# Optimization experiments

Hardware: AMD Instinct MI355X
Metric: run time of the kernel (lower is better)

## Reference

```python
import jax, jax.numpy as jnp
import numpy as np

D_MODEL = 1024
N_HEADS = 16
NUM_EXPERTS = 8
GATE_HIDDEN = 128
B, T = 4, 2048


def setup_inputs() -> dict:
    key = jax.random.key(0)
    ks = jax.random.split(key, 14)
    s = 0.02
    d, e, gh = D_MODEL, NUM_EXPERTS, GATE_HIDDEN
    return {
        "hidden_states": jax.random.normal(ks[0], (B, T, d), jnp.float32),
        # torch Linear weights are [out_features, in_features]
        "Wq": jax.random.normal(ks[1], (e, d, d), jnp.float32) * s,
        "bq": jax.random.normal(ks[2], (e, d), jnp.float32) * s,
        "Wk": jax.random.normal(ks[3], (e, d, d), jnp.float32) * s,
        "bk": jax.random.normal(ks[4], (e, d), jnp.float32) * s,
        "Wv": jax.random.normal(ks[5], (e, d, d), jnp.float32) * s,
        "bv": jax.random.normal(ks[6], (e, d), jnp.float32) * s,
        "Wg1": jax.random.normal(ks[7], (gh, d), jnp.float32) * s,
        "bg1": jax.random.normal(ks[8], (gh,), jnp.float32) * s,
        "Wg2": jax.random.normal(ks[9], (e, gh), jnp.float32) * s,
        "bg2": jax.random.normal(ks[10], (e,), jnp.float32) * s,
        "Wo": jax.random.normal(ks[11], (d, d), jnp.float32) * s,
        "bo": jax.random.normal(ks[12], (d,), jnp.float32) * s,
    }


def reference(hidden_states, Wq, bq, Wk, bk, Wv, bv, Wg1, bg1, Wg2, bg2, Wo, bo):
    Bb, Tt, C = hidden_states.shape
    H = N_HEADS
    Dh = C // H

    # Per-sample gating over mean-pooled sequence
    pooled = hidden_states.mean(axis=1)                        # [B, C]
    gate_h = jax.nn.relu(pooled @ Wg1.T + bg1)                 # [B, 128]
    gw = jax.nn.softmax(gate_h @ Wg2.T + bg2, axis=-1)         # [B, E]

    # Since gating weights are per-batch scalars, sum_e w_e * (x W_e^T + b_e)
    # == x (sum_e w_e W_e)^T + sum_e w_e b_e  — same math, one GEMM per sample.
    def proj(We, be):
        W_eff = jnp.einsum('be,eoi->boi', gw, We)              # [B, C, C]
        b_eff = gw @ be                                        # [B, C]
        y = jnp.einsum('bti,boi->bto', hidden_states, W_eff) + b_eff[:, None, :]
        return y.reshape(Bb, Tt, H, Dh).transpose(0, 2, 1, 3)  # [B, H, T, Dh]

    q = proj(Wq, bq)
    k = proj(Wk, bk)
    v = proj(Wv, bv)

    scores = jnp.einsum('bhtd,bhsd->bhts', q, k) / (Dh ** 0.5)
    attn = jax.nn.softmax(scores, axis=-1)                     # dropout is inference identity
    out = jnp.einsum('bhts,bhsd->bhtd', attn, v)
    out = out.transpose(0, 2, 1, 3).reshape(Bb, Tt, C)
    return out @ Wo.T + bo
```

## Files before the change

### kernel.cpp

```cpp
#include <hip/hip_runtime.h>

#define B_ 4
#define T_ 2048
#define C_ 1024
#define H_ 16
#define DH_ 64
#define E_ 8
#define GH_ 128

typedef unsigned short bf16_t;
typedef __attribute__((ext_vector_type(8))) __bf16 bf16x8;
typedef __attribute__((ext_vector_type(2))) __bf16 bf16x2;
typedef __attribute__((ext_vector_type(4))) float floatx4;

#if __has_builtin(__builtin_amdgcn_exp2f)
#define EXP2F(x) __builtin_amdgcn_exp2f(x)
#else
#define EXP2F(x) exp2f(x)
#endif

__device__ __forceinline__ bf16_t f2bf(float f) {
  unsigned int u = __builtin_bit_cast(unsigned int, f);
  u += 0x7fffu + ((u >> 16) & 1u);
  return (bf16_t)(u >> 16);
}
__device__ __forceinline__ void async16(const void* g, void* l) {
  __builtin_amdgcn_global_load_lds(
      (const __attribute__((address_space(1))) unsigned int*)g,
      (__attribute__((address_space(3))) unsigned int*)l, 16, 0, 0);
}

__global__ void cvt_kernel(const float* __restrict__ src, bf16_t* __restrict__ dst) {
  int i = (blockIdx.x * 256 + threadIdx.x) * 4;
  float4 v = *(const float4*)(src + i);
  bf16_t o4[4] = {f2bf(v.x), f2bf(v.y), f2bf(v.z), f2bf(v.w)};
  *(uint2*)(dst + i) = *(const uint2*)o4;
}

__global__ void pool_kernel(const float* __restrict__ x, float* __restrict__ partial) {
  int bz = blockIdx.x;
  int b = bz >> 4;
  int r0 = (bz & 15) * 128;
  int t = threadIdx.x;
  float a0 = 0.f, a1 = 0.f, a2 = 0.f, a3 = 0.f;
  const float* xb = x + (size_t)b * T_ * C_ + (size_t)r0 * C_;
  for (int r = 0; r < 128; ++r) {
    const float* row = xb + (size_t)r * C_;
    a0 += row[t]; a1 += row[t + 256]; a2 += row[t + 512]; a3 += row[t + 768];
  }
  float* p = partial + (size_t)bz * C_;
  p[t] = a0; p[t + 256] = a1; p[t + 512] = a2; p[t + 768] = a3;
}

__global__ void gate_kernel(const float* __restrict__ partial,
                            const float* __restrict__ Wg1, const float* __restrict__ bg1,
                            const float* __restrict__ Wg2, const float* __restrict__ bg2,
                            const float* __restrict__ bq, const float* __restrict__ bk,
                            const float* __restrict__ bv,
                            float* __restrict__ gw, float* __restrict__ beff) {
  int b = blockIdx.x;
  int t = threadIdx.x;
  __shared__ float spool[C_];
  __shared__ float sh[GH_];
  __shared__ float sgw[E_];
  for (int i = t; i < C_; i += GH_) {
    float s = 0.f;
    for (int j = 0; j < 16; ++j) s += partial[(size_t)(b * 16 + j) * C_ + i];
    spool[i] = s * (1.0f / T_);
  }
  __syncthreads();
  {
    float acc = 0.f;
    const float* wr = Wg1 + (size_t)t * C_;
    for (int i = 0; i < C_; i += 4) {
      float4 w = *(const float4*)(wr + i);
      acc += spool[i] * w.x + spool[i + 1] * w.y + spool[i + 2] * w.z + spool[i + 3] * w.w;
    }
    acc += bg1[t];
    sh[t] = fmaxf(acc, 0.0f);
  }
  __syncthreads();
  if (t < E_) {
    float acc = 0.f;
    const float* wr = Wg2 + t * GH_;
    for (int j = 0; j < GH_; ++j) acc += sh[j] * wr[j];
    sgw[t] = acc + bg2[t];
  }
  __syncthreads();
  if (t == 0) {
    float mx = sgw[0];
    for (int e = 1; e < E_; ++e) mx = fmaxf(mx, sgw[e]);
    float s = 0.f, ex[E_];
    for (int e = 0; e < E_; ++e) { ex[e] = __expf(sgw[e] - mx); s += ex[e]; }
    float inv = 1.0f / s;
    for (int e = 0; e < E_; ++e) { sgw[e] = ex[e] * inv; gw[b * E_ + e] = sgw[e]; }
  }
  __syncthreads();
  for (int o = t; o < C_; o += GH_) {
    float aq = 0.f, ak = 0.f, av = 0.f;
    #pragma unroll
    for (int e = 0; e < E_; ++e) {
      float w = sgw[e];
      aq += w * bq[e * C_ + o];
      ak += w * bk[e * C_ + o];
      av += w * bv[e * C_ + o];
    }
    beff[(0 * B_ + b) * C_ + o] = aq;
    beff[(1 * B_ + b) * C_ + o] = ak;
    beff[(2 * B_ + b) * C_ + o] = av;
  }
}

__global__ void combine_kernel(const float* __restrict__ Wq, const float* __restrict__ Wk,
                               const float* __restrict__ Wv, const float* __restrict__ gw,
                               bf16_t* __restrict__ Weff) {
  int g = blockIdx.x * 256 + threadIdx.x;
  int ig = (g & 127) * 8;
  int o = (g >> 7) & 1023;
  int p = g >> 17;
  const float* W = (p == 0) ? Wq : (p == 1) ? Wk : Wv;
  const float* src = W + (size_t)o * C_ + ig;
  float acc[B_][8];
  #pragma unroll
  for (int b = 0; b < B_; ++b)
    #pragma unroll
    for (int j = 0; j < 8; ++j) acc[b][j] = 0.f;
  #pragma unroll
  for (int e = 0; e < E_; ++e) {
    float4 lo = *(const float4*)(src + (size_t)e * C_ * C_);
    float4 hi = *(const float4*)(src + (size_t)e * C_ * C_ + 4);
    float w8[8] = {lo.x, lo.y, lo.z, lo.w, hi.x, hi.y, hi.z, hi.w};
    #pragma unroll
    for (int b = 0; b < B_; ++b) {
      float wgt = gw[b * E_ + e];
      #pragma unroll
      for (int j = 0; j < 8; ++j) acc[b][j] += wgt * w8[j];
    }
  }
  #pragma unroll
  for (int b = 0; b < B_; ++b) {
    bf16_t out8[8];
    #pragma unroll
    for (int j = 0; j < 8; ++j) out8[j] = f2bf(acc[b][j]);
    *(uint4*)(Weff + ((size_t)p * B_ + b) * C_ * C_ + (size_t)o * C_ + ig) = *(const uint4*)out8;
  }
}

template <int MODE>
__global__ __launch_bounds__(256) void gemm128(const bf16_t* __restrict__ X,
                                               const bf16_t* __restrict__ W,
                                               const float* __restrict__ bias,
                                               bf16_t* __restrict__ Yb,
                                               float* __restrict__ Yf) {
  if (MODE == 0) {
    int z = blockIdx.z;
    X += (size_t)(z & 3) * (T_ * C_);
    W += (size_t)z * (C_ * C_);
    bias += (size_t)z * C_;
    Yb += (size_t)z * (T_ * C_);
  }
  const int n0 = blockIdx.x * 128;
  const int m0 = blockIdx.y * 128;

  __shared__ __align__(16) bf16_t As[128][64];
  __shared__ __align__(16) bf16_t Bs[128][64];

  const int tid = threadIdx.x;
  const int wave = tid >> 6;
  const int lane = tid & 63;
  const int quad = lane >> 4;
  const int l16 = lane & 15;
  const int wm = (wave & 1) * 64;
  const int wn = (wave >> 1) * 64;

  floatx4 acc[4][4];
  #pragma unroll
  for (int i = 0; i < 4; ++i)
    #pragma unroll
    for (int j = 0; j < 4; ++j) { floatx4 zz = {0.f, 0.f, 0.f, 0.f}; acc[i][j] = zz; }

  const int ar = tid >> 3;
  const int ac = (tid & 7) * 8;
  const bf16_t* Xp = X + (size_t)(m0 + ar) * C_ + ac;
  const bf16_t* Wp = W + (size_t)(n0 + ar) * C_ + ac;

  for (int k0 = 0; k0 < C_; k0 += 64) {
    __syncthreads();
    #pragma unroll
    for (int s = 0; s < 4; ++s) {
      async16(Xp + (size_t)(s * 32) * C_ + k0, &As[ar + s * 32][ac]);
      async16(Wp + (size_t)(s * 32) * C_ + k0, &Bs[ar + s * 32][ac]);
    }
    __syncthreads();
    #pragma unroll
    for (int kk = 0; kk < 64; kk += 32) {
      bf16x8 af[4], bfr[4];
      #pragma unroll
      for (int i = 0; i < 4; ++i) {
        af[i] = *(const bf16x8*)(&As[wm + i * 16 + l16][kk + quad * 8]);
        bfr[i] = *(const bf16x8*)(&Bs[wn + i * 16 + l16][kk + quad * 8]);
      }
      #pragma unroll
      for (int mi = 0; mi < 4; ++mi)
        #pragma unroll
        for (int ni = 0; ni < 4; ++ni)
          acc[mi][ni] = __builtin_amdgcn_mfma_f32_16x16x32_bf16(af[mi], bfr[ni], acc[mi][ni], 0, 0, 0);
    }
  }

  #pragma unroll
  for (int mi = 0; mi < 4; ++mi) {
    #pragma unroll
    for (int ni = 0; ni < 4; ++ni) {
      const int n = n0 + wn + ni * 16 + l16;
      const float bv = bias[n];
      #pragma unroll
      for (int r = 0; r < 4; ++r) {
        const int m = m0 + wm + mi * 16 + quad * 4 + r;
        float v = acc[mi][ni][r] + bv;
        if (MODE == 0) Yb[((size_t)(n >> 6) * T_ + m) * DH_ + (n & 63)] = f2bf(v);
        else           Yf[(size_t)m * C_ + n] = v;
      }
    }
  }
}

__global__ void vtrans_kernel(const bf16_t* __restrict__ qkv, bf16_t* __restrict__ Vt) {
  const int kt = blockIdx.x;
  const int bh = blockIdx.y;
  const int b = bh >> 4, h = bh & 15;
  const bf16_t* src = qkv + (size_t)(8 + b) * T_ * C_ + (size_t)h * T_ * DH_ + (size_t)kt * 64 * DH_;
  __shared__ __align__(16) bf16_t L[64][64];
  const int t = threadIdx.x;
  const int r = t >> 2;
  const int c = (t & 3) * 16;
  const int sw = r & 48;
  *(uint4*)(&L[r][c ^ sw]) = *(const uint4*)(src + (size_t)r * DH_ + c);
  *(uint4*)(&L[r][(c ^ sw) + 8]) = *(const uint4*)(src + (size_t)r * DH_ + c + 8);
  __syncthreads();
  const int sw2 = c & 48;
  bf16_t tmp[16];
  #pragma unroll
  for (int j = 0; j < 16; ++j) tmp[j] = L[c + j][r ^ sw2];
  bf16_t* dst = Vt + (size_t)bh * DH_ * T_ + (size_t)r * T_ + (size_t)kt * 64 + c;
  *(uint4*)(dst) = *(const uint4*)(tmp);
  *(uint4*)(dst + 8) = *(const uint4*)(tmp + 8);
}

__global__ __launch_bounds__(512, 4) void attn_kernel(const bf16_t* __restrict__ qkv,
                                                      const bf16_t* __restrict__ Vt,
                                                      bf16_t* __restrict__ out) {
  const int bh = blockIdx.x;
  const int qt = blockIdx.y;
  const int b = bh >> 4, h = bh & 15;
  const __bf16* Q = (const __bf16*)(qkv + (size_t)b * T_ * C_ + (size_t)h * T_ * DH_);
  const bf16_t* Kp = qkv + (size_t)(4 + b) * T_ * C_ + (size_t)h * T_ * DH_;
  const bf16_t* Vtb = Vt + (size_t)bh * DH_ * T_;

  __shared__ __align__(16) bf16_t Ks[512 * 8];
  __shared__ __align__(16) bf16_t Vs[512 * 8];
  __shared__ __align__(16) __bf16 Ps[128][72];

  const int tid = threadIdx.x;
  const int wave = tid >> 6;
  const int lane = tid & 63;
  const int quad = lane >> 4;
  const int l16 = lane & 15;

  const float QSC = 0.125f * 1.44269504f;
  bf16x8 qb[2];
  {
    const __bf16* qrow = Q + (size_t)(qt * 128 + wave * 16 + l16) * DH_;
    #pragma unroll
    for (int kc = 0; kc < 2; ++kc) {
      union { bf16x8 v; __bf16 e[8]; } fr;
      #pragma unroll
      for (int j = 0; j < 8; ++j) fr.e[j] = (__bf16)((float)qrow[kc * 32 + quad * 8 + j] * QSC);
      qb[kc] = fr.v;
    }
  }

  int kaoff[2][4];
  int vboff[2][4];
  #pragma unroll
  for (int kc = 0; kc < 2; ++kc) {
    #pragma unroll
    for (int i = 0; i < 4; ++i) {
      int row = i * 16 + l16;
      int off = ((row << 3) + (((kc << 2) + quad) ^ (row & 7))) * 8;
      kaoff[kc][i] = off;
      vboff[kc][i] = off;
    }
  }
  __bf16* prow = &Ps[wave * 16 + l16][0];
  const bf16x8* paptr0 = (const bf16x8*)(prow + 0 * 32 + quad * 8);
  const bf16x8* paptr1 = (const bf16x8*)(prow + 1 * 32 + quad * 8);

  floatx4 oacc[4];
  #pragma unroll
  for (int di = 0; di < 4; ++di) { floatx4 zz = {0.f, 0.f, 0.f, 0.f}; oacc[di] = zz; }
  float lrun = 0.f;

  const int srow = tid >> 3;
  const int schk = (tid & 7) ^ (srow & 7);

  for (int kt = 0; kt < T_ / 64; ++kt) {
    const int kv0 = kt * 64;
    __syncthreads();
    async16(Kp + (size_t)(kv0 + srow) * DH_ + schk * 8, Ks + (size_t)tid * 8);
    async16(Vtb + (size_t)srow * T_ + kv0 + schk * 8, Vs + (size_t)tid * 8);
    __syncthreads();

    floatx4 s_[4];
    #pragma unroll
    for (int ni = 0; ni < 4; ++ni) { floatx4 zz = {0.f, 0.f, 0.f, 0.f}; s_[ni] = zz; }
    #pragma unroll
    for (int kc = 0; kc < 2; ++kc) {
      #pragma unroll
      for (int ni = 0; ni < 4; ++ni) {
        bf16x8 ka = *(const bf16x8*)(Ks + kaoff[kc][ni]);
        s_[ni] = __builtin_amdgcn_mfma_f32_16x16x32_bf16(ka, qb[kc], s_[ni], 0, 0, 0);
      }
    }

    float lsum = 0.f;
    #pragma unroll
    for (int ni = 0; ni < 4; ++ni) {
      float p0 = EXP2F(s_[ni][0]);
      float p1 = EXP2F(s_[ni][1]);
      float p2 = EXP2F(s_[ni][2]);
      float p3 = EXP2F(s_[ni][3]);
      lsum += (p0 + p1) + (p2 + p3);
      bf16x2 w0 = {(__bf16)p0, (__bf16)p1};
      bf16x2 w1 = {(__bf16)p2, (__bf16)p3};
      uint2 pk;
      pk.x = __builtin_bit_cast(unsigned int, w0);
      pk.y = __builtin_bit_cast(unsigned int, w1);
      *(uint2*)(prow + ni * 16 + quad * 4) = pk;
    }
    lsum += __shfl_xor(lsum, 16);
    lsum += __shfl_xor(lsum, 32);
    lrun += lsum;

    #pragma unroll
    for (int kc = 0; kc < 2; ++kc) {
      bf16x8 pa = *(kc == 0 ? paptr0 : paptr1);
      #pragma unroll
      for (int di = 0; di < 4; ++di) {
        bf16x8 vb = *(const bf16x8*)(Vs + vboff[kc][di]);
        oacc[di] = __builtin_amdgcn_mfma_f32_16x16x32_bf16(pa, vb, oacc[di], 0, 0, 0);
      }
    }
  }

  float linv = 1.0f / lrun;
  #pragma unroll
  for (int r = 0; r < 4; ++r) {
    float li = __shfl(linv, quad * 20 + r);
    int m = qt * 128 + wave * 16 + quad * 4 + r;
    #pragma unroll
    for (int di = 0; di < 4; ++di) {
      int d = di * 16 + l16;
      out[(size_t)b * T_ * C_ + (size_t)m * C_ + h * DH_ + d] = f2bf(oacc[di][r] * li);
    }
  }
}

extern "C" void kernel_launch(void* const* d_in, const int* in_sizes, int n_in,
                              void* d_out, int out_size, void* d_ws, size_t ws_size,
                              hipStream_t stream) {
  (void)in_sizes; (void)n_in; (void)out_size; (void)ws_size;
  const float* x   = (const float*)d_in[0];
  const float* Wq  = (const float*)d_in[1];
  const float* bq  = (const float*)d_in[2];
  const float* Wk  = (const float*)d_in[3];
  const float* bk  = (const float*)d_in[4];
  const float* Wv  = (const float*)d_in[5];
  const float* bv  = (const float*)d_in[6];
  const float* Wg1 = (const float*)d_in[7];
  const float* bg1 = (const float*)d_in[8];
  const float* Wg2 = (const float*)d_in[9];
  const float* bg2 = (const float*)d_in[10];
  const float* Wo  = (const float*)d_in[11];
  const float* bo  = (const float*)d_in[12];

  char* ws = (char*)d_ws;
  size_t off = 0;
  auto alloc = [&](size_t bytes) -> void* {
    void* p = ws + off;
    off += (bytes + 255) & ~(size_t)255;
    return p;
  };
  float* partial = (float*)alloc((size_t)B_ * 16 * C_ * 4);
  float* gw      = (float*)alloc((size_t)B_ * E_ * 4);
  float* beff    = (float*)alloc((size_t)3 * B_ * C_ * 4);
  bf16_t* xbf    = (bf16_t*)alloc((size_t)B_ * T_ * C_ * 2);
  bf16_t* Wobf   = (bf16_t*)alloc((size_t)C_ * C_ * 2);
  bf16_t* Weff   = (bf16_t*)alloc((size_t)3 * B_ * C_ * C_ * 2);
  bf16_t* qkv    = (bf16_t*)alloc((size_t)3 * B_ * T_ * C_ * 2);
  bf16_t* attn   = (bf16_t*)alloc((size_t)B_ * T_ * C_ * 2);
  bf16_t* Vt = xbf;

  pool_kernel<<<dim3(B_ * 16), 256, 0, stream>>>(x, partial);
  gate_kernel<<<dim3(B_), GH_, 0, stream>>>(partial, Wg1, bg1, Wg2, bg2,
                                            bq, bk, bv, gw, beff);
  combine_kernel<<<dim3(3 * C_ * (C_ / 8) / 256), 256, 0, stream>>>(Wq, Wk, Wv, gw, Weff);
  cvt_kernel<<<dim3((B_ * T_ * C_) / 1024), 256, 0, stream>>>(x, xbf);
  cvt_kernel<<<dim3((C_ * C_) / 1024), 256, 0, stream>>>(Wo, Wobf);
  gemm128<0><<<dim3(C_ / 128, T_ / 128, 12), 256, 0, stream>>>(xbf, Weff, beff, qkv, nullptr);
  vtrans_kernel<<<dim3(T_ / 64, B_ * H_), 256, 0, stream>>>(qkv, Vt);
  attn_kernel<<<dim3(B_ * H_, T_ / 128), 512, 0, stream>>>(qkv, Vt, attn);
  gemm128<1><<<dim3(C_ / 128, (B_ * T_) / 128, 1), 256, 0, stream>>>(attn, Wobf, bo, nullptr, (float*)d_out);
}
```

Measured before the change: 450.7 us.

## Double-buffer K/V tiles in attention with async prefetch and wave priority

The attention kernel now keeps two LDS buffers for K and V and issues the async load of the next 64-key tile before computing on the current one, waiting with s_waitcnt vmcnt instead of a full sync. The goal is to hide global-load latency behind the MFMA and softmax work. It also raises wave priority around the MFMA sections and changes the launch bounds to 6 blocks per CU. The extra LDS and the occupancy hint may pressure registers or LDS capacity, so fewer blocks could actually fit per CU.

```diff
diff --git a/kernel.cpp b/kernel.cpp
--- a/kernel.cpp
+++ b/kernel.cpp
@@ -247,7 +247,7 @@
   *(uint4*)(dst + 8) = *(const uint4*)(tmp + 8);
 }
 
-__global__ __launch_bounds__(512, 4) void attn_kernel(const bf16_t* __restrict__ qkv,
+__global__ __launch_bounds__(512, 6) void attn_kernel(const bf16_t* __restrict__ qkv,
                                                       const bf16_t* __restrict__ Vt,
                                                       bf16_t* __restrict__ out) {
   const int bh = blockIdx.x;
@@ -257,8 +257,8 @@
   const bf16_t* Kp = qkv + (size_t)(4 + b) * T_ * C_ + (size_t)h * T_ * DH_;
   const bf16_t* Vtb = Vt + (size_t)bh * DH_ * T_;
 
-  __shared__ __align__(16) bf16_t Ks[512 * 8];
-  __shared__ __align__(16) bf16_t Vs[512 * 8];
+  __shared__ __align__(16) bf16_t Ks[2][4096];
+  __shared__ __align__(16) bf16_t Vs[2][4096];
   __shared__ __align__(16) __bf16 Ps[128][72];
 
   const int tid = threadIdx.x;
@@ -280,16 +280,13 @@
     }
   }
 
-  int kaoff[2][4];
-  int vboff[2][4];
+  int off_[2][4];
   #pragma unroll
   for (int kc = 0; kc < 2; ++kc) {
     #pragma unroll
     for (int i = 0; i < 4; ++i) {
       int row = i * 16 + l16;
-      int off = ((row << 3) + (((kc << 2) + quad) ^ (row & 7))) * 8;
-      kaoff[kc][i] = off;
-      vboff[kc][i] = off;
+      off_[kc][i] = ((row << 3) + (((kc << 2) + quad) ^ (row & 7))) * 8;
     }
   }
   __bf16* prow = &Ps[wave * 16 + l16][0];
@@ -303,55 +300,91 @@
 
   const int srow = tid >> 3;
   const int schk = (tid & 7) ^ (srow & 7);
-
-  for (int kt = 0; kt < T_ / 64; ++kt) {
-    const int kv0 = kt * 64;
-    __syncthreads();
-    async16(Kp + (size_t)(kv0 + srow) * DH_ + schk * 8, Ks + (size_t)tid * 8);
-    async16(Vtb + (size_t)srow * T_ + kv0 + schk * 8, Vs + (size_t)tid * 8);
-    __syncthreads();
-
-    floatx4 s_[4];
-    #pragma unroll
-    for (int ni = 0; ni < 4; ++ni) { floatx4 zz = {0.f, 0.f, 0.f, 0.f}; s_[ni] = zz; }
-    #pragma unroll
-    for (int kc = 0; kc < 2; ++kc) {
-      #pragma unroll
-      for (int ni = 0; ni < 4; ++ni) {
-        bf16x8 ka = *(const bf16x8*)(Ks + kaoff[kc][ni]);
-        s_[ni] = __builtin_amdgcn_mfma_f32_16x16x32_bf16(ka, qb[kc], s_[ni], 0, 0, 0);
-      }
-    }
-
-    float lsum = 0.f;
-    #pragma unroll
-    for (int ni = 0; ni < 4; ++ni) {
-      float p0 = EXP2F(s_[ni][0]);
-      float p1 = EXP2F(s_[ni][1]);
-      float p2 = EXP2F(s_[ni][2]);
-      float p3 = EXP2F(s_[ni][3]);
-      lsum += (p0 + p1) + (p2 + p3);
-      bf16x2 w0 = {(__bf16)p0, (__bf16)p1};
-      bf16x2 w1 = {(__bf16)p2, (__bf16)p3};
-      uint2 pk;
-      pk.x = __builtin_bit_cast(unsigned int, w0);
-      pk.y = __builtin_bit_cast(unsigned int, w1);
-      *(uint2*)(prow + ni * 16 + quad * 4) = pk;
-    }
-    lsum += __shfl_xor(lsum, 16);
-    lsum += __shfl_xor(lsum, 32);
-    lrun += lsum;
-
-    #pragma unroll
-    for (int kc = 0; kc < 2; ++kc) {
-      bf16x8 pa = *(kc == 0 ? paptr0 : paptr1);
-      #pragma unroll
-      for (int di = 0; di < 4; ++di) {
-        bf16x8 vb = *(const bf16x8*)(Vs + vboff[kc][di]);
-        oacc[di] = __builtin_amdgcn_mfma_f32_16x16x32_bf16(pa, vb, oacc[di], 0, 0, 0);
-      }
-    }
-  }
+  const bf16_t* kg = Kp + (size_t)srow * DH_ + schk * 8;
+  const bf16_t* vg = Vtb + (size_t)srow * T_ + schk * 8;
+
+#define STAGE(BUF) do {                                   \
+    async16(kg, &Ks[BUF][tid * 8]);                       \
+    async16(vg, &Vs[BUF][tid * 8]);                       \
+    kg += 64 * DH_;                                       \
+    vg += 64;                                             \
+  } while (0)
+
+#define WAITV(N) asm volatile("s_waitcnt vmcnt(" #N ")" ::: "memory")
+#define BAR() __builtin_amdgcn_s_barrier()
+
+#define COMPUTE(CUR) do {                                                            \
+    floatx4 s_[4];                                                                   \
+    _Pragma("unroll")                                                                \
+    for (int ni = 0; ni < 4; ++ni) { floatx4 zz = {0.f, 0.f, 0.f, 0.f}; s_[ni] = zz; } \
+    __builtin_amdgcn_s_setprio(1);                                                   \
+    _Pragma("unroll")                                                                \
+    for (int kc = 0; kc < 2; ++kc) {                                                 \
+      _Pragma("unroll")                                                              \
+      for (int ni = 0; ni < 4; ++ni) {                                               \
+        bf16x8 ka = *(const bf16x8*)(&Ks[CUR][off_[kc][ni]]);                        \
+        s_[ni] = __builtin_amdgcn_mfma_f32_16x16x32_bf16(ka, qb[kc], s_[ni], 0, 0, 0); \
+      }                                                                              \
+    }                                                                                \
+    __builtin_amdgcn_s_setprio(0);                                                   \
+    float lsum = 0.f;                                                                \
+    _Pragma("unroll")                                                                \
+    for (int ni = 0; ni < 4; ++ni) {                                                 \
+      float p0 = EXP2F(s_[ni][0]);                                                   \
+      float p1 = EXP2F(s_[ni][1]);                                                   \
+      float p2 = EXP2F(s_[ni][2]);                                                   \
+      float p3 = EXP2F(s_[ni][3]);                                                   \
+      lsum += (p0 + p1) + (p2 + p3);                                                 \
+      bf16x2 w0 = {(__bf16)p0, (__bf16)p1};                                          \
+      bf16x2 w1 = {(__bf16)p2, (__bf16)p3};                                          \
+      uint2 pk;                                                                      \
+      pk.x = __builtin_bit_cast(unsigned int, w0);                                   \
+      pk.y = __builtin_bit_cast(unsigned int, w1);                                   \
+      *(uint2*)(prow + ni * 16 + quad * 4) = pk;                                     \
+    }                                                                                \
+    lsum += __shfl_xor(lsum, 16);                                                    \
+    lsum += __shfl_xor(lsum, 32);                                                    \
+    lrun += lsum;                                                                    \
+    __builtin_amdgcn_s_setprio(1);                                                   \
+    _Pragma("unroll")                                                                \
+    for (int kc = 0; kc < 2; ++kc) {                                                 \
+      bf16x8 pa = *(kc == 0 ? paptr0 : paptr1);                                      \
+      _Pragma("unroll")                                                              \
+      for (int di = 0; di < 4; ++di) {                                               \
+        bf16x8 vb = *(const bf16x8*)(&Vs[CUR][off_[kc][di]]);                        \
+        oacc[di] = __builtin_amdgcn_mfma_f32_16x16x32_bf16(pa, vb, oacc[di], 0, 0, 0); \
+      }                                                                              \
+    }                                                                                \
+    __builtin_amdgcn_s_setprio(0);                                                   \
+  } while (0)
+
+  STAGE(0);
+  #pragma unroll 1
+  for (int kt = 0; kt < 30; kt += 2) {
+    STAGE(1);
+    WAITV(2);
+    BAR();
+    COMPUTE(0);
+    BAR();
+    STAGE(0);
+    WAITV(2);
+    BAR();
+    COMPUTE(1);
+    BAR();
+  }
+  STAGE(1);
+  WAITV(2);
+  BAR();
+  COMPUTE(0);
+  BAR();
+  WAITV(0);
+  BAR();
+  COMPUTE(1);
+
+#undef STAGE
+#undef WAITV
+#undef BAR
+#undef COMPUTE
 
   float linv = 1.0f / lrun;
   #pragma unroll
```

After: 453.6 us. About the same (+0.6%).
